# Performance work log

Measured on AMD Instinct MI355X. Metric: run time of the kernel, lower is better.

Reference implementation:

```python
import jax, jax.numpy as jnp
import numpy as np

B, S, UNITS = 32, 2048, 512
D = 2 * UNITS  # 1024


def setup_inputs() -> dict:
    key = jax.random.key(0)
    ks = jax.random.split(key, 12)
    s = 1.0 / np.sqrt(D)
    mask = (jax.random.uniform(ks[0], (B, S)) < 0.9).astype(jnp.float32)
    mask = mask.at[:, 0].set(1.0)  # guarantee no all-zero row
    return {
        "dec_hidden": jax.random.normal(ks[1], (2, B, UNITS), dtype=jnp.float32),
        "enc_output": jax.random.normal(ks[2], (B, S, D), dtype=jnp.float32),
        "enc_pad_mask": mask,
        "prev_coverage": jax.random.uniform(ks[3], (B, S), dtype=jnp.float32) * 0.1,
        "Wh": jax.random.uniform(ks[4], (D, D), minval=-s, maxval=s),
        "bh": jax.random.uniform(ks[5], (D,), minval=-s, maxval=s),
        "Ws": jax.random.uniform(ks[6], (D, D), minval=-s, maxval=s),
        "bs": jax.random.uniform(ks[7], (D,), minval=-s, maxval=s),
        "Wc": jax.random.uniform(ks[8], (D, 1), minval=-1.0, maxval=1.0),
        "bc": jax.random.uniform(ks[9], (D,), minval=-1.0, maxval=1.0),
        "v": jax.random.uniform(ks[10], (1, D), minval=-s, maxval=s),
        "bv": jax.random.uniform(ks[11], (1,), minval=-s, maxval=s),
        "use_coverage": 1,
    }


def reference(dec_hidden, enc_output, enc_pad_mask, prev_coverage,
              Wh, bh, Ws, bs, Wc, bc, v, bv, use_coverage):
    # dec_hidden: (2, B, units) -> (B, 1, 2*units)
    dec = jnp.transpose(dec_hidden, (1, 0, 2)).reshape(dec_hidden.shape[1], 1, -1)
    enc_features = jnp.einsum('bsd,ed->bse', enc_output, Wh) + bh  # (B,S,D)
    dec_features = jnp.einsum('bod,ed->boe', dec, Ws) + bs          # (B,1,D)
    att_inputs = enc_features + dec_features
    if use_coverage:
        # Linear(1 -> D) applied to prev_coverage[..., None]
        coverage_features = prev_coverage[:, :, None] * Wc[:, 0][None, None, :] + bc
        att_inputs = att_inputs + coverage_features
    score = jnp.einsum('bsd,od->bso', jnp.tanh(att_inputs), v) + bv  # (B,S,1)
    attention_weights = jax.nn.softmax(score, axis=1)[..., 0]        # (B,S)
    attention_weights = attention_weights * enc_pad_mask
    attention_weights = attention_weights / jnp.sum(attention_weights, axis=1, keepdims=True)
    context_vector = jnp.einsum('bs,bsd->bd', attention_weights, enc_output)
    if use_coverage:
        coverage_vector = prev_coverage + attention_weights
        return context_vector, attention_weights, coverage_vector
    return context_vector, attention_weights
```

## Files before the change

kernel.cpp:

```cpp
#include <hip/hip_runtime.h>
#include <hip/hip_bf16.h>

#define BATCH 32
#define SEQ   2048
#define DIM   1024

typedef __attribute__((ext_vector_type(4))) float f32x4;
typedef __attribute__((ext_vector_type(8))) short short8;

static __device__ __forceinline__ ushort f2bf(float x) {
    __hip_bfloat16 h = __float2bfloat16(x);
    union { __hip_bfloat16 h; ushort u; } cv; cv.h = h;
    return cv.u;
}
static __device__ __forceinline__ float bf2f(ushort u) {
    union { unsigned int i; float f; } cv; cv.i = ((unsigned int)u) << 16;
    return cv.f;
}

static __device__ __forceinline__ void gll16(const void* g, void* l) {
    __builtin_amdgcn_global_load_lds(
        (const __attribute__((address_space(1))) void*)g,
        (__attribute__((address_space(3))) void*)l, 16, 0, 0);
}

__global__ __launch_bounds__(256) void kAPack(const float* __restrict__ enc,
                                              ushort* __restrict__ apk) {
    int g = blockIdx.x * 256 + threadIdx.x;
    int lane = g & 63;
    int fr   = (g >> 6) & 15;
    int S    = (g >> 10) & 31;
    int strip = g >> 15;
    int row = (strip << 8) + (fr << 4) + (lane & 15);
    int k0  = (S << 5) + ((lane >> 4) << 3);
    const float* src = enc + (size_t)row * DIM + k0;
    float4 a = *(const float4*)src;
    float4 b = *(const float4*)(src + 4);
    union { ushort us[8]; uint4 u4; } pk;
    pk.us[0] = f2bf(a.x); pk.us[1] = f2bf(a.y); pk.us[2] = f2bf(a.z); pk.us[3] = f2bf(a.w);
    pk.us[4] = f2bf(b.x); pk.us[5] = f2bf(b.y); pk.us[6] = f2bf(b.z); pk.us[7] = f2bf(b.w);
    *(uint4*)(apk + (size_t)g * 8) = pk.u4;
}

__global__ __launch_bounds__(256) void kWhPack(const float* __restrict__ Wh,
                                               ushort* __restrict__ bpk) {
    int g = blockIdx.x * 256 + threadIdx.x;
    int lane = g & 63;
    int fr   = (g >> 6) & 15;
    int S    = (g >> 10) & 31;
    int nb   = g >> 15;
    int e  = (nb << 8) + (fr << 4) + (lane & 15);
    int k0 = (S << 5) + ((lane >> 4) << 3);
    const float* src = Wh + (size_t)e * DIM + k0;
    float4 a = *(const float4*)src;
    float4 b = *(const float4*)(src + 4);
    union { ushort us[8]; uint4 u4; } pk;
    pk.us[0] = f2bf(a.x); pk.us[1] = f2bf(a.y); pk.us[2] = f2bf(a.z); pk.us[3] = f2bf(a.w);
    pk.us[4] = f2bf(b.x); pk.us[5] = f2bf(b.y); pk.us[6] = f2bf(b.z); pk.us[7] = f2bf(b.w);
    *(uint4*)(bpk + (size_t)g * 8) = pk.u4;
}

__global__ __launch_bounds__(256) void kBase(const float* __restrict__ dh,
                                             const float* __restrict__ Ws,
                                             const float* __restrict__ bs,
                                             const float* __restrict__ bh,
                                             const float* __restrict__ bc,
                                             const int* __restrict__ uc,
                                             float* __restrict__ base) {
    __shared__ float dec[8][DIM];
    int ec = blockIdx.x >> 2;
    int bg = blockIdx.x & 3;
    int b0 = bg * 8, e0 = ec * 32;
    int tid = threadIdx.x;
    for (int i = tid; i < 8 * DIM; i += 256) {
        int bb = i >> 10, d = i & 1023;
        float vdec = (d < 512) ? dh[(b0 + bb) * 512 + d]
                               : dh[BATCH * 512 + (b0 + bb) * 512 + d - 512];
        dec[bb][d] = vdec;
    }
    __syncthreads();
    int el = tid >> 3, ds = tid & 7;
    int e = e0 + el;
    float acc[8] = {0.f, 0.f, 0.f, 0.f, 0.f, 0.f, 0.f, 0.f};
    const float* wrow = Ws + (size_t)e * DIM;
    for (int i = 0; i < 128; ++i) {
        int d = i * 8 + ds;
        float wv = wrow[d];
#pragma unroll
        for (int bb = 0; bb < 8; ++bb) acc[bb] += wv * dec[bb][d];
    }
#pragma unroll
    for (int bb = 0; bb < 8; ++bb) {
        float s = acc[bb];
        s += __shfl_xor(s, 1); s += __shfl_xor(s, 2); s += __shfl_xor(s, 4);
        acc[bb] = s;
    }
    if (ds == 0) {
        float bias = bs[e] + bh[e] + ((*uc) ? bc[e] : 0.0f);
#pragma unroll
        for (int bb = 0; bb < 8; ++bb) base[(b0 + bb) * DIM + e] = acc[bb] + bias;
    }
}

__global__ __launch_bounds__(256, 4) void kScore(const ushort* __restrict__ apk,
                                                 const ushort* __restrict__ bpk,
                                                 const float* __restrict__ base,
                                                 const float* __restrict__ pc,
                                                 const float* __restrict__ Wc,
                                                 const float* __restrict__ vv,
                                                 const int* __restrict__ uc,
                                                 float* __restrict__ scorep) {
    __shared__ ushort Al[2][4096];
    __shared__ ushort Bl[2][4096];

    const int tid = threadIdx.x;
    const int w = tid >> 6, lane = tid & 63;
    const int q = lane >> 4, l15 = lane & 15;
    const int wm = w >> 1, wn = w & 1;

    const int x = blockIdx.x & 7;
    const int j = blockIdx.x >> 3;
    const int ms = (x << 6) + (j >> 3);
    const int np = j & 7;
    const int b = ms >> 4;
    const int s0 = (ms & 15) << 7;

    const ushort* pa = apk + ((size_t)(ms >> 1) << 18)
                     + ((size_t)(((ms & 1) << 3) + (w << 1)) << 9) + (lane << 3);
    const ushort* pb = bpk + ((size_t)(np >> 1) << 18)
                     + ((size_t)(((np & 1) << 3) + (w << 1)) << 9) + (lane << 3);
    ushort* da0 = &Al[0][(w << 1) << 9];
    ushort* da1 = &Al[1][(w << 1) << 9];
    ushort* db0 = &Bl[0][(w << 1) << 9];
    ushort* db1 = &Bl[1][(w << 1) << 9];

#define STG(DA, DB) do { \
    gll16(pa, (DA)); gll16(pa + 512, (DA) + 512); \
    gll16(pb, (DB)); gll16(pb + 512, (DB) + 512); \
    pa += 8192; pb += 8192; \
} while (0)

    f32x4 acc[4][4] = {};

#define CMP(BUF) do { \
    short8 a_[4], b_[4]; \
    _Pragma("unroll") \
    for (int mf = 0; mf < 4; ++mf) \
        a_[mf] = *(const short8*)&Al[BUF][(((wm << 2) + mf) << 9) + (lane << 3)]; \
    _Pragma("unroll") \
    for (int ef = 0; ef < 4; ++ef) \
        b_[ef] = *(const short8*)&Bl[BUF][(((wn << 2) + ef) << 9) + (lane << 3)]; \
    _Pragma("unroll") \
    for (int ef = 0; ef < 4; ++ef) \
        _Pragma("unroll") \
        for (int mf = 0; mf < 4; ++mf) \
            acc[mf][ef] = __builtin_amdgcn_mfma_f32_16x16x32_bf16(a_[mf], b_[ef], acc[mf][ef], 0, 0, 0); \
} while (0)

    STG(da0, db0);
    __syncthreads();

    for (int it = 0; it < 16; ++it) {
        STG(da1, db1);
        CMP(0);
        __syncthreads();
        if (it < 15) STG(da0, db0);
        CMP(1);
        __syncthreads();
    }

    float* red = (float*)&Al[0][0];
    const float ucf = (float)(*uc);
    float basee[4], ve[4], wce[4];
#pragma unroll
    for (int ef = 0; ef < 4; ++ef) {
        int e = (np << 7) + (wn << 6) + (ef << 4) + l15;
        basee[ef] = base[b * DIM + e];
        ve[ef] = vv[e];
        wce[ef] = Wc[e] * ucf;
    }
#pragma unroll
    for (int mf = 0; mf < 4; ++mf) {
#pragma unroll
        for (int r = 0; r < 4; ++r) {
            int rl = (wm << 6) + (mf << 4) + (q << 2) + r;
            float p = pc[b * SEQ + s0 + rl];
            float sp = 0.f;
#pragma unroll
            for (int ef = 0; ef < 4; ++ef) {
                float xv = acc[mf][ef][r] + basee[ef] + p * wce[ef];
                float tt = 1.0f - 2.0f / (1.0f + __expf(2.0f * xv));
                sp += tt * ve[ef];
            }
            sp += __shfl_xor(sp, 1);
            sp += __shfl_xor(sp, 2);
            sp += __shfl_xor(sp, 4);
            sp += __shfl_xor(sp, 8);
            if (l15 == 0) red[(wn << 7) + rl] = sp;
        }
    }
    __syncthreads();
    if (tid < 128)
        scorep[np * (BATCH * SEQ) + b * SEQ + s0 + tid] = red[tid] + red[128 + tid];
}

__global__ __launch_bounds__(512) void kSoftmax(const float* __restrict__ scorep,
                                                const float* __restrict__ mask,
                                                const float* __restrict__ pc,
                                                float* __restrict__ att,
                                                float* __restrict__ cov,
                                                int write_cov) {
    __shared__ float rmax[8], rsum[8];
    const int BS = BATCH * SEQ;
    int b = blockIdx.x, tid = threadIdx.x;
    int wv = tid >> 6, ln = tid & 63;
    float x[4];
#pragma unroll
    for (int i = 0; i < 4; ++i) {
        int idx = b * SEQ + tid + i * 512;
        float s01 = scorep[idx] + scorep[BS + idx];
        float s23 = scorep[2 * BS + idx] + scorep[3 * BS + idx];
        float s45 = scorep[4 * BS + idx] + scorep[5 * BS + idx];
        float s67 = scorep[6 * BS + idx] + scorep[7 * BS + idx];
        x[i] = (s01 + s23) + (s45 + s67);
    }
    float m = fmaxf(fmaxf(x[0], x[1]), fmaxf(x[2], x[3]));
#pragma unroll
    for (int o = 1; o < 64; o <<= 1) m = fmaxf(m, __shfl_xor(m, o));
    if (ln == 0) rmax[wv] = m;
    __syncthreads();
    m = rmax[0];
#pragma unroll
    for (int i = 1; i < 8; ++i) m = fmaxf(m, rmax[i]);

    float ms[4], wm[4];
#pragma unroll
    for (int i = 0; i < 4; ++i) ms[i] = mask[b * SEQ + tid + i * 512];
    float s = 0.f;
#pragma unroll
    for (int i = 0; i < 4; ++i) { wm[i] = __expf(x[i] - m) * ms[i]; s += wm[i]; }
#pragma unroll
    for (int o = 1; o < 64; o <<= 1) s += __shfl_xor(s, o);
    if (ln == 0) rsum[wv] = s;
    __syncthreads();
    s = 0.f;
#pragma unroll
    for (int i = 0; i < 8; ++i) s += rsum[i];
    float inv = 1.0f / s;
#pragma unroll
    for (int i = 0; i < 4; ++i) {
        float wf = wm[i] * inv;
        att[b * SEQ + tid + i * 512] = wf;
        if (write_cov) cov[b * SEQ + tid + i * 512] = pc[b * SEQ + tid + i * 512] + wf;
    }
}

__global__ __launch_bounds__(256) void kCtxPart(const ushort* __restrict__ apk,
                                                const float* __restrict__ att,
                                                float* __restrict__ part) {
    __shared__ float attl[256];
    const int strip = blockIdx.x;
    const int tid = threadIdx.x;
    const int wv = tid >> 6, l = tid & 63;
    const int q = l >> 4, l15 = l & 15;
    attl[tid] = att[(strip << 8) + tid];
    __syncthreads();

    const ushort* sb = apk + ((size_t)strip << 18);
#pragma unroll
    for (int c = 0; c < 8; ++c) {
        int S = (wv << 3) + c;
        const ushort* kbase = sb + ((size_t)S << 13) + (l << 3);
        float a8[8] = {0.f, 0.f, 0.f, 0.f, 0.f, 0.f, 0.f, 0.f};
#pragma unroll
        for (int fr = 0; fr < 16; ++fr) {
            short8 v = *(const short8*)(kbase + (fr << 9));
            float wgt = attl[(fr << 4) + l15];
#pragma unroll
            for (int jj = 0; jj < 8; ++jj) a8[jj] += wgt * bf2f((ushort)v[jj]);
        }
#pragma unroll
        for (int o = 1; o < 16; o <<= 1)
#pragma unroll
            for (int jj = 0; jj < 8; ++jj) a8[jj] += __shfl_xor(a8[jj], o);
        if (l15 == 0) {
            int d0 = (S << 5) + (q << 3);
            float* dst = part + ((size_t)strip << 10) + d0;
#pragma unroll
            for (int jj = 0; jj < 8; ++jj) dst[jj] = a8[jj];
        }
    }
}

__global__ __launch_bounds__(256) void kCtxReduce(const float* __restrict__ part,
                                                  float* __restrict__ ctx) {
    int g = blockIdx.x * 256 + threadIdx.x;
    int b = g >> 10, d = g & 1023;
    float s = 0.f;
#pragma unroll
    for (int i = 0; i < 8; ++i) s += part[((size_t)((b << 3) + i) << 10) + d];
    ctx[g] = s;
}

extern "C" void kernel_launch(void* const* d_in, const int* in_sizes, int n_in,
                              void* d_out, int out_size, void* d_ws, size_t ws_size,
                              hipStream_t stream) {
    const float* dh   = (const float*)d_in[0];
    const float* enc  = (const float*)d_in[1];
    const float* mask = (const float*)d_in[2];
    const float* pc   = (const float*)d_in[3];
    const float* Wh   = (const float*)d_in[4];
    const float* bh   = (const float*)d_in[5];
    const float* Ws   = (const float*)d_in[6];
    const float* bs   = (const float*)d_in[7];
    const float* Wc   = (const float*)d_in[8];
    const float* bc   = (const float*)d_in[9];
    const float* vv   = (const float*)d_in[10];
    const int* uc     = (const int*)d_in[12];

    float* ctx = (float*)d_out;
    float* att = ctx + BATCH * DIM;
    float* cov = att + BATCH * SEQ;
    int write_cov = (out_size >= BATCH * (DIM + 2 * SEQ)) ? 1 : 0;

    ushort* apk  = (ushort*)d_ws;
    ushort* bpk  = apk + (size_t)BATCH * SEQ * DIM;
    float* base   = (float*)(bpk + (size_t)DIM * DIM);
    float* scorep = base + BATCH * DIM;
    float* part   = scorep + 8 * BATCH * SEQ;

    kAPack<<<32768, 256, 0, stream>>>(enc, apk);
    kWhPack<<<512, 256, 0, stream>>>(Wh, bpk);
    kBase<<<128, 256, 0, stream>>>(dh, Ws, bs, bh, bc, uc, base);
    kScore<<<4096, 256, 0, stream>>>(apk, bpk, base, pc, Wc, vv, uc, scorep);
    kSoftmax<<<BATCH, 512, 0, stream>>>(scorep, mask, pc, att, cov, write_cov);
    kCtxPart<<<256, 256, 0, stream>>>(apk, att, part);
    kCtxReduce<<<128, 256, 0, stream>>>(part, ctx);
}
```

Measured before the change: 312.2 us.

## Enlarge kScore GEMM tile to 256x256 with phased LDS pipeline and fewer partials

The score GEMM block tile grows from 128x128 to 256x256 with 512 threads (8 waves, 2x4 layout) and 32 accumulators per wave. This raises arithmetic intensity and cuts the score partial planes from 8 to 4. The main loop is rebuilt as four phases per K-tile, each with an explicit barrier, a waitcnt and s_setprio around the MFMA bursts, interleaving global-to-LDS staging with compute. The risks are heavier register and LDS pressure (about 130KB LDS, so one block per CU) and the hand-tuned waitcnt counts.

```diff
diff --git a/kernel.cpp b/kernel.cpp
--- a/kernel.cpp
+++ b/kernel.cpp
@@ -102,7 +102,7 @@
     }
 }
 
-__global__ __launch_bounds__(256, 4) void kScore(const ushort* __restrict__ apk,
+__global__ __launch_bounds__(512, 2) void kScore(const ushort* __restrict__ apk,
                                                  const ushort* __restrict__ bpk,
                                                  const float* __restrict__ base,
                                                  const float* __restrict__ pc,
@@ -110,80 +110,118 @@
                                                  const float* __restrict__ vv,
                                                  const int* __restrict__ uc,
                                                  float* __restrict__ scorep) {
-    __shared__ ushort Al[2][4096];
-    __shared__ ushort Bl[2][4096];
+    __shared__ ushort Al[2][16384];
+    __shared__ ushort Bl[2][16384];
+    __shared__ float red[4][256];
 
     const int tid = threadIdx.x;
     const int w = tid >> 6, lane = tid & 63;
     const int q = lane >> 4, l15 = lane & 15;
-    const int wm = w >> 1, wn = w & 1;
+    const int wm = w >> 2, wn = w & 3;
 
     const int x = blockIdx.x & 7;
     const int j = blockIdx.x >> 3;
-    const int ms = (x << 6) + (j >> 3);
-    const int np = j & 7;
-    const int b = ms >> 4;
-    const int s0 = (ms & 15) << 7;
-
-    const ushort* pa = apk + ((size_t)(ms >> 1) << 18)
-                     + ((size_t)(((ms & 1) << 3) + (w << 1)) << 9) + (lane << 3);
-    const ushort* pb = bpk + ((size_t)(np >> 1) << 18)
-                     + ((size_t)(((np & 1) << 3) + (w << 1)) << 9) + (lane << 3);
-    ushort* da0 = &Al[0][(w << 1) << 9];
-    ushort* da1 = &Al[1][(w << 1) << 9];
-    ushort* db0 = &Bl[0][(w << 1) << 9];
-    ushort* db1 = &Bl[1][(w << 1) << 9];
-
-#define STG(DA, DB) do { \
-    gll16(pa, (DA)); gll16(pa + 512, (DA) + 512); \
-    gll16(pb, (DB)); gll16(pb + 512, (DB) + 512); \
-    pa += 8192; pb += 8192; \
-} while (0)
-
-    f32x4 acc[4][4] = {};
-
-#define CMP(BUF) do { \
-    short8 a_[4], b_[4]; \
-    _Pragma("unroll") \
-    for (int mf = 0; mf < 4; ++mf) \
-        a_[mf] = *(const short8*)&Al[BUF][(((wm << 2) + mf) << 9) + (lane << 3)]; \
-    _Pragma("unroll") \
-    for (int ef = 0; ef < 4; ++ef) \
-        b_[ef] = *(const short8*)&Bl[BUF][(((wn << 2) + ef) << 9) + (lane << 3)]; \
-    _Pragma("unroll") \
-    for (int ef = 0; ef < 4; ++ef) \
-        _Pragma("unroll") \
-        for (int mf = 0; mf < 4; ++mf) \
-            acc[mf][ef] = __builtin_amdgcn_mfma_f32_16x16x32_bf16(a_[mf], b_[ef], acc[mf][ef], 0, 0, 0); \
-} while (0)
-
-    STG(da0, db0);
-    __syncthreads();
-
-    for (int it = 0; it < 16; ++it) {
-        STG(da1, db1);
-        CMP(0);
-        __syncthreads();
-        if (it < 15) STG(da0, db0);
-        CMP(1);
-        __syncthreads();
-    }
-
-    float* red = (float*)&Al[0][0];
+    const int ms = (x << 5) + (j >> 2);
+    const int nbk = j & 3;
+    const int b = ms >> 3;
+    const int s0 = (ms & 7) << 8;
+
+    const ushort* pa = apk + ((size_t)ms << 18) + ((w << 1) << 9) + (lane << 3);
+    const ushort* pb = bpk + ((size_t)nbk << 18) + ((w << 1) << 9) + (lane << 3);
+
+    f32x4 acc[8][4] = {};
+
+#define LDA(BUF, MH, MF, KB) \
+    (*(const short8*)&Al[BUF][((((((wm << 3) + ((MH) << 2) + (MF)) << 1) + (KB)) << 9)) + (lane << 3)])
+#define LDB(BUF, EF, KB) \
+    (*(const short8*)&Bl[BUF][((((((wn << 2) + (EF)) << 1) + (KB)) << 9)) + (lane << 3)])
+
+#define STG_A(TN, NB, KB) do { \
+    const ushort* s_ = pa + ((size_t)(((TN) << 1) + (KB)) << 13); \
+    gll16(s_,       &Al[NB][((((w << 1) << 1) + (KB)) << 9)]); \
+    gll16(s_ + 512, &Al[NB][(((((w << 1) + 1) << 1) + (KB)) << 9)]); \
+} while (0)
+#define STG_B(TN, NB, KB) do { \
+    const ushort* s_ = pb + ((size_t)(((TN) << 1) + (KB)) << 13); \
+    gll16(s_,       &Bl[NB][((((w << 1) << 1) + (KB)) << 9)]); \
+    gll16(s_ + 512, &Bl[NB][(((((w << 1) + 1) << 1) + (KB)) << 9)]); \
+} while (0)
+#define STG_NONE ((void)0)
+
+#define MFMA16(MH, KB) do { \
+    __builtin_amdgcn_s_setprio(1); \
+    acc[(MH)*4+0][0] = __builtin_amdgcn_mfma_f32_16x16x32_bf16(a0, b0, acc[(MH)*4+0][0], 0, 0, 0); \
+    acc[(MH)*4+1][0] = __builtin_amdgcn_mfma_f32_16x16x32_bf16(a1, b0, acc[(MH)*4+1][0], 0, 0, 0); \
+    acc[(MH)*4+2][0] = __builtin_amdgcn_mfma_f32_16x16x32_bf16(a2, b0, acc[(MH)*4+2][0], 0, 0, 0); \
+    acc[(MH)*4+3][0] = __builtin_amdgcn_mfma_f32_16x16x32_bf16(a3, b0, acc[(MH)*4+3][0], 0, 0, 0); \
+    acc[(MH)*4+0][1] = __builtin_amdgcn_mfma_f32_16x16x32_bf16(a0, b1, acc[(MH)*4+0][1], 0, 0, 0); \
+    acc[(MH)*4+1][1] = __builtin_amdgcn_mfma_f32_16x16x32_bf16(a1, b1, acc[(MH)*4+1][1], 0, 0, 0); \
+    acc[(MH)*4+2][1] = __builtin_amdgcn_mfma_f32_16x16x32_bf16(a2, b1, acc[(MH)*4+2][1], 0, 0, 0); \
+    acc[(MH)*4+3][1] = __builtin_amdgcn_mfma_f32_16x16x32_bf16(a3, b1, acc[(MH)*4+3][1], 0, 0, 0); \
+    acc[(MH)*4+0][2] = __builtin_amdgcn_mfma_f32_16x16x32_bf16(a0, b2, acc[(MH)*4+0][2], 0, 0, 0); \
+    acc[(MH)*4+1][2] = __builtin_amdgcn_mfma_f32_16x16x32_bf16(a1, b2, acc[(MH)*4+1][2], 0, 0, 0); \
+    acc[(MH)*4+2][2] = __builtin_amdgcn_mfma_f32_16x16x32_bf16(a2, b2, acc[(MH)*4+2][2], 0, 0, 0); \
+    acc[(MH)*4+3][2] = __builtin_amdgcn_mfma_f32_16x16x32_bf16(a3, b2, acc[(MH)*4+3][2], 0, 0, 0); \
+    acc[(MH)*4+0][3] = __builtin_amdgcn_mfma_f32_16x16x32_bf16(a0, b3, acc[(MH)*4+0][3], 0, 0, 0); \
+    acc[(MH)*4+1][3] = __builtin_amdgcn_mfma_f32_16x16x32_bf16(a1, b3, acc[(MH)*4+1][3], 0, 0, 0); \
+    acc[(MH)*4+2][3] = __builtin_amdgcn_mfma_f32_16x16x32_bf16(a2, b3, acc[(MH)*4+2][3], 0, 0, 0); \
+    acc[(MH)*4+3][3] = __builtin_amdgcn_mfma_f32_16x16x32_bf16(a3, b3, acc[(MH)*4+3][3], 0, 0, 0); \
+    __builtin_amdgcn_s_setprio(0); \
+} while (0)
+
+#define PHASE(BUF, MH, KB, STG, WAITN) do { \
+    short8 a0 = LDA(BUF, MH, 0, KB), a1 = LDA(BUF, MH, 1, KB); \
+    short8 a2 = LDA(BUF, MH, 2, KB), a3 = LDA(BUF, MH, 3, KB); \
+    short8 b0 = LDB(BUF, 0, KB), b1 = LDB(BUF, 1, KB); \
+    short8 b2 = LDB(BUF, 2, KB), b3 = LDB(BUF, 3, KB); \
+    STG; \
+    __builtin_amdgcn_s_barrier(); \
+    asm volatile("s_waitcnt lgkmcnt(0)" ::: "memory"); \
+    __builtin_amdgcn_sched_barrier(0); \
+    MFMA16(MH, KB); \
+    if ((WAITN) == 2) { asm volatile("s_waitcnt vmcnt(2)" ::: "memory"); } \
+    if ((WAITN) == 0) { asm volatile("s_waitcnt vmcnt(0)" ::: "memory"); } \
+    __builtin_amdgcn_s_barrier(); \
+} while (0)
+
+#define TILE(BUF, NB, TN) do { \
+    PHASE(BUF, 0, 0, STG_A(TN, NB, 0), 2); \
+    PHASE(BUF, 0, 1, STG_A(TN, NB, 1), -1); \
+    PHASE(BUF, 1, 0, STG_B(TN, NB, 0), -1); \
+    PHASE(BUF, 1, 1, STG_B(TN, NB, 1), 2); \
+} while (0)
+#define TILE_LAST(BUF) do { \
+    PHASE(BUF, 0, 0, STG_NONE, 0); \
+    PHASE(BUF, 0, 1, STG_NONE, -1); \
+    PHASE(BUF, 1, 0, STG_NONE, -1); \
+    PHASE(BUF, 1, 1, STG_NONE, -1); \
+} while (0)
+
+    STG_A(0, 0, 0); STG_A(0, 0, 1); STG_B(0, 0, 0); STG_B(0, 0, 1);
+    asm volatile("s_waitcnt vmcnt(0)" ::: "memory");
+    __builtin_amdgcn_s_barrier();
+
+    for (int t2 = 0; t2 < 7; ++t2) {
+        TILE(0, 1, 2 * t2 + 1);
+        TILE(1, 0, 2 * t2 + 2);
+    }
+    TILE(0, 1, 15);
+    TILE_LAST(1);
+
     const float ucf = (float)(*uc);
     float basee[4], ve[4], wce[4];
 #pragma unroll
     for (int ef = 0; ef < 4; ++ef) {
-        int e = (np << 7) + (wn << 6) + (ef << 4) + l15;
+        int e = (nbk << 8) + ((wn << 2) + ef) * 16 + l15;
         basee[ef] = base[b * DIM + e];
         ve[ef] = vv[e];
         wce[ef] = Wc[e] * ucf;
     }
 #pragma unroll
-    for (int mf = 0; mf < 4; ++mf) {
+    for (int mf = 0; mf < 8; ++mf) {
 #pragma unroll
         for (int r = 0; r < 4; ++r) {
-            int rl = (wm << 6) + (mf << 4) + (q << 2) + r;
+            int rl = (wm << 7) + (mf << 4) + (q << 2) + r;
             float p = pc[b * SEQ + s0 + rl];
             float sp = 0.f;
 #pragma unroll
@@ -196,12 +234,14 @@
             sp += __shfl_xor(sp, 2);
             sp += __shfl_xor(sp, 4);
             sp += __shfl_xor(sp, 8);
-            if (l15 == 0) red[(wn << 7) + rl] = sp;
+            if (l15 == 0) red[wn][rl] = sp;
         }
     }
     __syncthreads();
-    if (tid < 128)
-        scorep[np * (BATCH * SEQ) + b * SEQ + s0 + tid] = red[tid] + red[128 + tid];
+    if (tid < 256) {
+        float s = (red[0][tid] + red[1][tid]) + (red[2][tid] + red[3][tid]);
+        scorep[nbk * (BATCH * SEQ) + b * SEQ + s0 + tid] = s;
+    }
 }
 
 __global__ __launch_bounds__(512) void kSoftmax(const float* __restrict__ scorep,
@@ -218,11 +258,7 @@
 #pragma unroll
     for (int i = 0; i < 4; ++i) {
         int idx = b * SEQ + tid + i * 512;
-        float s01 = scorep[idx] + scorep[BS + idx];
-        float s23 = scorep[2 * BS + idx] + scorep[3 * BS + idx];
-        float s45 = scorep[4 * BS + idx] + scorep[5 * BS + idx];
-        float s67 = scorep[6 * BS + idx] + scorep[7 * BS + idx];
-        x[i] = (s01 + s23) + (s45 + s67);
+        x[i] = (scorep[idx] + scorep[BS + idx]) + (scorep[2 * BS + idx] + scorep[3 * BS + idx]);
     }
     float m = fmaxf(fmaxf(x[0], x[1]), fmaxf(x[2], x[3]));
 #pragma unroll
@@ -327,12 +363,12 @@
     ushort* bpk  = apk + (size_t)BATCH * SEQ * DIM;
     float* base   = (float*)(bpk + (size_t)DIM * DIM);
     float* scorep = base + BATCH * DIM;
-    float* part   = scorep + 8 * BATCH * SEQ;
+    float* part   = scorep + 4 * BATCH * SEQ;
 
     kAPack<<<32768, 256, 0, stream>>>(enc, apk);
     kWhPack<<<512, 256, 0, stream>>>(Wh, bpk);
     kBase<<<128, 256, 0, stream>>>(dh, Ws, bs, bh, bc, uc, base);
-    kScore<<<4096, 256, 0, stream>>>(apk, bpk, base, pc, Wc, vv, uc, scorep);
+    kScore<<<1024, 512, 0, stream>>>(apk, bpk, base, pc, Wc, vv, uc, scorep);
     kSoftmax<<<BATCH, 512, 0, stream>>>(scorep, mask, pc, att, cov, write_cov);
     kCtxPart<<<256, 256, 0, stream>>>(apk, att, part);
     kCtxReduce<<<128, 256, 0, stream>>>(part, ctx);
```

New measurement: 317.2 us. No clear change (+1.6%).
